# Optimization experiments

Measured on AMD Instinct MI355X. Metric: run time of the kernel, lower is better.

The kernel has to match this reference:

```python
import jax, jax.numpy as jnp
import numpy as np

N_POINTS = 16384
N_SAMPLES = 8192


def setup_inputs() -> dict:
    key = jax.random.key(0)
    k1, k2, k3, k4 = jax.random.split(key, 4)
    a = jax.random.normal(k1, (3, N_POINTS), dtype=jnp.float32)
    b = jax.random.normal(k2, (3, N_POINTS), dtype=jnp.float32)
    # stand-ins for np.random.shuffle(...)[:n_samples] in the torch forward
    a_idx = jax.random.randint(k3, (N_SAMPLES,), 0, N_POINTS, dtype=jnp.int64)
    b_idx = jax.random.randint(k4, (N_SAMPLES,), 0, N_POINTS, dtype=jnp.int64)
    return {"a": a, "b": b, "a_idx": a_idx, "b_idx": b_idx}


def reference(a, b, a_idx, b_idx):
    # a, b: [3, N]; sample n_samples columns, transpose -> [n, 3], keep xyz
    pa = a[:, a_idx].T[:, :3]  # [n, 3]
    pb = b[:, b_idx].T[:, :3]  # [n, 3]
    # d[k, i] = ||pa_i - pb_k||^2, via ||a||^2 + ||b||^2 - 2 b.a^T
    # (avoids the original's [n, n, 3] broadcasted difference tensor)
    sq_a = jnp.sum(pa * pa, axis=1)  # [n]
    sq_b = jnp.sum(pb * pb, axis=1)  # [n]
    d = sq_a[None, :] + sq_b[:, None] - 2.0 * (pb @ pa.T)  # [n, n]
    # torch.min(d, 0)[0].sum(): min over b-points for each a-point, then sum
    return jnp.min(d, axis=0).sum()
```

## Files before the change

### kernel.cpp

```cpp
#include <hip/hip_runtime.h>
#include <stdint.h>


#define BLOCK   256
#define NPTS_A  4
#define BPTS    128

__global__ __launch_bounds__(BLOCK)
void chamfer_pack_kernel(const float* __restrict__ a,
                         const float* __restrict__ b,
                         const int* __restrict__ a_idx,
                         const int* __restrict__ b_idx,
                         float4* __restrict__ pa4,
                         float4* __restrict__ pb4,
                         int N, int n) {
    int i = blockIdx.x * BLOCK + threadIdx.x;
    if (i < n) {
        int ai = a_idx[i];
        float x = a[ai], y = a[N + ai], z = a[2 * N + ai];
        pa4[i] = make_float4(x, y, z, x * x + y * y + z * z);
        int bi = b_idx[i];
        float u = b[bi], v = b[N + bi], w = b[2 * N + bi];
        pb4[i] = make_float4(-2.f * u, -2.f * v, -2.f * w,
                             u * u + v * v + w * w);
    }
}

__global__ __launch_bounds__(BLOCK)
void chamfer_min_kernel(const float4* __restrict__ pa4,
                        const float4* __restrict__ pb4,
                        float* __restrict__ pmin,
                        int n, int a_chunks) {
    __shared__ float4 tile[BPTS];
    const int bid = blockIdx.x;
    const int ac  = bid % a_chunks;
    const int bc  = bid / a_chunks;
    const int tid = threadIdx.x;

    if (tid < BPTS)
        tile[tid] = pb4[bc * BPTS + tid];
    __syncthreads();

    float ax[NPTS_A], ay[NPTS_A], az[NPTS_A], mn[NPTS_A];
#pragma unroll
    for (int m = 0; m < NPTS_A; ++m) {
        int i = ac * (BLOCK * NPTS_A) + m * BLOCK + tid;
        float4 p = pa4[i];
        ax[m] = p.x; ay[m] = p.y; az[m] = p.z;
        mn[m] = 3.4e38f;
    }

#pragma unroll 4
    for (int k = 0; k < BPTS; ++k) {
        float4 t = tile[k];
#pragma unroll
        for (int m = 0; m < NPTS_A; ++m) {
            float c = fmaf(t.x, ax[m], fmaf(t.y, ay[m], fmaf(t.z, az[m], t.w)));
            mn[m] = fminf(mn[m], c);
        }
    }

#pragma unroll
    for (int m = 0; m < NPTS_A; ++m) {
        int i = ac * (BLOCK * NPTS_A) + m * BLOCK + tid;
        pmin[(size_t)bc * n + i] = mn[m];
    }
}

__global__ __launch_bounds__(BLOCK)
void chamfer_colmin_sum_kernel(const float4* __restrict__ pa4,
                               const float* __restrict__ pmin,
                               float* __restrict__ psum,
                               int n, int b_chunks) {
    __shared__ float wsum[BLOCK / 64];
    const int tid = threadIdx.x;
    const int i = blockIdx.x * BLOCK + tid;

    float v = 3.4e38f;
#pragma unroll 8
    for (int j = 0; j < b_chunks; ++j)
        v = fminf(v, pmin[(size_t)j * n + i]);

    v += pa4[i].w;

#pragma unroll
    for (int off = 32; off > 0; off >>= 1)
        v += __shfl_down(v, off, 64);
    if ((tid & 63) == 0) wsum[tid >> 6] = v;
    __syncthreads();
    if (tid == 0) {
        float s = 0.f;
#pragma unroll
        for (int w = 0; w < BLOCK / 64; ++w) s += wsum[w];
        psum[blockIdx.x] = s;
    }
}

__global__ __launch_bounds__(64)
void chamfer_final_kernel(const float* __restrict__ psum,
                          float* __restrict__ out, int nblocks) {
    const int tid = threadIdx.x;
    float v = (tid < nblocks) ? psum[tid] : 0.f;
#pragma unroll
    for (int off = 32; off > 0; off >>= 1)
        v += __shfl_down(v, off, 64);
    if (tid == 0) out[0] = v;
}

extern "C" void kernel_launch(void* const* d_in, const int* in_sizes, int n_in,
                              void* d_out, int out_size, void* d_ws, size_t ws_size,
                              hipStream_t stream) {
    const float* a     = (const float*)d_in[0];
    const float* b     = (const float*)d_in[1];
    const int*   a_idx = (const int*)d_in[2];
    const int*   b_idx = (const int*)d_in[3];
    float*       out   = (float*)d_out;

    const int N = in_sizes[0] / 3;
    const int n = in_sizes[2];

    const int a_chunks = n / (BLOCK * NPTS_A);
    const int b_chunks = n / BPTS;
    const int nblocks2 = n / BLOCK;

    float4* pa4  = (float4*)d_ws;
    float4* pb4  = pa4 + n;
    float*  pmin = (float*)(pb4 + n);
    float*  psum = pmin + (size_t)b_chunks * n;

    chamfer_pack_kernel<<<(n + BLOCK - 1) / BLOCK, BLOCK, 0, stream>>>(
        a, b, a_idx, b_idx, pa4, pb4, N, n);

    chamfer_min_kernel<<<a_chunks * b_chunks, BLOCK, 0, stream>>>(
        pa4, pb4, pmin, n, a_chunks);

    chamfer_colmin_sum_kernel<<<nblocks2, BLOCK, 0, stream>>>(
        pa4, pmin, psum, n, b_chunks);

    chamfer_final_kernel<<<1, 64, 0, stream>>>(psum, out, nblocks2);
}
```

Baseline: 75.64 us.

## Replace partial-min buffer with encoded atomicMin and atomic final sum

The min kernel no longer writes a b_chunks x n partial-min matrix. Each block now folds its per-point minima into one n-length array with atomicMin on an order-preserving unsigned encoding of the float. The final sum uses atomicAdd into the output, which drops the separate final-reduction launch, and the b-tile shrinks to 64 points to double the block count. In exchange there is more atomic traffic, the float summation order is no longer deterministic, and each block has less work to hide its load latency.

```diff
diff --git a/kernel.cpp b/kernel.cpp
--- a/kernel.cpp
+++ b/kernel.cpp
@@ -4,7 +4,16 @@
 
 #define BLOCK   256
 #define NPTS_A  4
-#define BPTS    128
+#define BPTS    64
+
+__device__ __forceinline__ unsigned enc_f32(float f) {
+    unsigned u = __float_as_uint(f);
+    return (u & 0x80000000u) ? ~u : (u | 0x80000000u);
+}
+__device__ __forceinline__ float dec_f32(unsigned u) {
+    return (u & 0x80000000u) ? __uint_as_float(u & 0x7FFFFFFFu)
+                             : __uint_as_float(~u);
+}
 
 __global__ __launch_bounds__(BLOCK)
 void chamfer_pack_kernel(const float* __restrict__ a,
@@ -13,6 +22,8 @@
                          const int* __restrict__ b_idx,
                          float4* __restrict__ pa4,
                          float4* __restrict__ pb4,
+                         unsigned* __restrict__ minarr,
+                         float* __restrict__ out,
                          int N, int n) {
     int i = blockIdx.x * BLOCK + threadIdx.x;
     if (i < n) {
@@ -23,14 +34,16 @@
         float u = b[bi], v = b[N + bi], w = b[2 * N + bi];
         pb4[i] = make_float4(-2.f * u, -2.f * v, -2.f * w,
                              u * u + v * v + w * w);
+        minarr[i] = 0xFFFFFFFFu;
     }
+    if (i == 0) out[0] = 0.f;
 }
 
 __global__ __launch_bounds__(BLOCK)
 void chamfer_min_kernel(const float4* __restrict__ pa4,
                         const float4* __restrict__ pb4,
-                        float* __restrict__ pmin,
-                        int n, int a_chunks) {
+                        unsigned* __restrict__ minarr,
+                        int a_chunks) {
     __shared__ float4 tile[BPTS];
     const int bid = blockIdx.x;
     const int ac  = bid % a_chunks;
@@ -50,7 +63,7 @@
         mn[m] = 3.4e38f;
     }
 
-#pragma unroll 4
+#pragma unroll 8
     for (int k = 0; k < BPTS; ++k) {
         float4 t = tile[k];
 #pragma unroll
@@ -63,25 +76,19 @@
 #pragma unroll
     for (int m = 0; m < NPTS_A; ++m) {
         int i = ac * (BLOCK * NPTS_A) + m * BLOCK + tid;
-        pmin[(size_t)bc * n + i] = mn[m];
+        atomicMin(&minarr[i], enc_f32(mn[m]));
     }
 }
 
 __global__ __launch_bounds__(BLOCK)
-void chamfer_colmin_sum_kernel(const float4* __restrict__ pa4,
-                               const float* __restrict__ pmin,
-                               float* __restrict__ psum,
-                               int n, int b_chunks) {
+void chamfer_reduce_kernel(const float4* __restrict__ pa4,
+                           const unsigned* __restrict__ minarr,
+                           float* __restrict__ out) {
     __shared__ float wsum[BLOCK / 64];
     const int tid = threadIdx.x;
     const int i = blockIdx.x * BLOCK + tid;
 
-    float v = 3.4e38f;
-#pragma unroll 8
-    for (int j = 0; j < b_chunks; ++j)
-        v = fminf(v, pmin[(size_t)j * n + i]);
-
-    v += pa4[i].w;
+    float v = dec_f32(minarr[i]) + pa4[i].w;
 
 #pragma unroll
     for (int off = 32; off > 0; off >>= 1)
@@ -92,19 +99,8 @@
         float s = 0.f;
 #pragma unroll
         for (int w = 0; w < BLOCK / 64; ++w) s += wsum[w];
-        psum[blockIdx.x] = s;
+        atomicAdd(out, s);
     }
-}
-
-__global__ __launch_bounds__(64)
-void chamfer_final_kernel(const float* __restrict__ psum,
-                          float* __restrict__ out, int nblocks) {
-    const int tid = threadIdx.x;
-    float v = (tid < nblocks) ? psum[tid] : 0.f;
-#pragma unroll
-    for (int off = 32; off > 0; off >>= 1)
-        v += __shfl_down(v, off, 64);
-    if (tid == 0) out[0] = v;
 }
 
 extern "C" void kernel_launch(void* const* d_in, const int* in_sizes, int n_in,
@@ -121,21 +117,17 @@
 
     const int a_chunks = n / (BLOCK * NPTS_A);
     const int b_chunks = n / BPTS;
-    const int nblocks2 = n / BLOCK;
 
-    float4* pa4  = (float4*)d_ws;
-    float4* pb4  = pa4 + n;
-    float*  pmin = (float*)(pb4 + n);
-    float*  psum = pmin + (size_t)b_chunks * n;
+    float4*   pa4    = (float4*)d_ws;
+    float4*   pb4    = pa4 + n;
+    unsigned* minarr = (unsigned*)(pb4 + n);
 
-    chamfer_pack_kernel<<<(n + BLOCK - 1) / BLOCK, BLOCK, 0, stream>>>(
-        a, b, a_idx, b_idx, pa4, pb4, N, n);
+    chamfer_pack_kernel<<<n / BLOCK, BLOCK, 0, stream>>>(
+        a, b, a_idx, b_idx, pa4, pb4, minarr, out, N, n);
 
     chamfer_min_kernel<<<a_chunks * b_chunks, BLOCK, 0, stream>>>(
-        pa4, pb4, pmin, n, a_chunks);
+        pa4, pb4, minarr, a_chunks);
 
-    chamfer_colmin_sum_kernel<<<nblocks2, BLOCK, 0, stream>>>(
-        pa4, pmin, psum, n, b_chunks);
-
-    chamfer_final_kernel<<<1, 64, 0, stream>>>(psum, out, nblocks2);
+    chamfer_reduce_kernel<<<n / BLOCK, BLOCK, 0, stream>>>(
+        pa4, minarr, out);
 }
```

Result: faster. 69.73 us (-7.8%).
